# Performance work log

Hardware: AMD Instinct MI355X
Metric: run time of the kernel (lower is better)

Reference implementation:

```python
import itertools
import jax, jax.numpy as jnp
import numpy as np

GAMMA = 1.0

def setup_inputs() -> dict:
    key = jax.random.key(0)
    ks = jax.random.split(key, 11)
    B, T, NP, NG, J, H = 16, 32, 8, 4, 14, 256
    return {
        'hor_heatmap': jax.random.normal(ks[0], (B, T, 1, H, H), jnp.float32),
        'hor_offset': jax.random.normal(ks[1], (B, T, NP, 2), jnp.float32),
        'hor_bsize': jax.random.normal(ks[2], (B, T, NP, 4), jnp.float32),
        'hor_center': jax.random.normal(ks[3], (B, T, NP, 2), jnp.float32),
        'scores': jax.random.uniform(ks[4], (B, T, NP), jnp.float32),
        'x_pose3d': jax.random.normal(ks[5], (B, T, NP, J, 3), jnp.float32),
        'gt_heatmap': jax.random.normal(ks[6], (B, T, H, H), jnp.float32),
        'gt_hor_boxes_wh': jax.random.normal(ks[7], (B, T, NG, 4), jnp.float32),
        'gt_hor_offset': jax.random.normal(ks[8], (B, T, NG, 2), jnp.float32),
        'gt_hor_center': jax.random.normal(ks[9], (B, T, NG, 2), jnp.float32),
        'gt_pose3d': jax.random.normal(ks[10], (B, T, NG, J, 3), jnp.float32),
    }

def _make_perms(num_pred, num_gt):
    # all injective assignments of each gt column to a distinct pred row
    return np.asarray(list(itertools.permutations(range(num_pred), num_gt)), dtype=np.int32)

def _match(cost, perms):
    # cost: [NP, NG]; perms: [P, NG] static. Exact linear_sum_assignment by enumeration.
    ng = cost.shape[1]
    totals = cost[perms, jnp.arange(ng)].sum(-1)  # [P]
    return perms[jnp.argmin(totals)]              # rows matched to cols 0..NG-1

def reference(hor_heatmap, hor_offset, hor_bsize, hor_center, scores, x_pose3d,
              gt_heatmap, gt_hor_boxes_wh, gt_hor_offset, gt_hor_center, gt_pose3d):
    B, T, NP, _ = hor_center.shape
    NG = gt_hor_center.shape[2]
    J = x_pose3d.shape[3]
    BT = B * T
    perms = jnp.asarray(_make_perms(NP, NG))

    # center loss: MSE mean over full heatmaps
    center_loss = jnp.mean((hor_heatmap[:, :, 0] - gt_heatmap) ** 2)

    # --- Hungarian box/offset losses, vmapped over (b,t) ---
    def per_bt_box(pc, gc, sc, po, go, ps, gs):
        # cost[i,j] = -score[i] + ||pc_i - gc_j||
        C = jnp.linalg.norm(pc[:, None] - gc[None], axis=-1) - sc[:, None]  # [NP,NG]
        rows = _match(C, perms)                                             # [NG]
        off = jnp.mean(jnp.abs(po[rows] - go), axis=-1).sum()   # L1 mean per pair, summed
        size = jnp.mean(jnp.abs(ps[rows] - gs), axis=-1).sum()
        return off, size

    flat = lambda x: x.reshape((BT,) + x.shape[2:])
    offs, sizes = jax.vmap(per_bt_box)(
        flat(hor_center), flat(gt_hor_center), flat(scores),
        flat(hor_offset), flat(gt_hor_offset), flat(hor_bsize), flat(gt_hor_boxes_wh))
    total_offset_loss = offs.sum() / BT
    total_size_loss = sizes.sum() / BT

    # --- Hungarian pose loss ---
    def per_bt_pose(pp, gp):
        d = pp[:, None] - gp[None]                       # [NP,NG,J,3]
        C = jnp.sqrt(jnp.sum(d * d, axis=(-1, -2)))      # Frobenius norm cost
        rows = _match(C, perms)
        return jnp.sum((pp[rows] - gp) ** 2)             # MSE(sum) per pair, summed

    pose_loss = jax.vmap(per_bt_pose)(flat(x_pose3d), flat(gt_pose3d)).sum() / (BT * NP * J)

    detection_loss = center_loss + total_offset_loss + total_size_loss
    return GAMMA * detection_loss + pose_loss
```

## Files before the change

### kernel.cpp

```cpp
#include <hip/hip_runtime.h>

#define BT      512
#define NP      8
#define NG      4
#define JNT     14
#define NCENTER 33554432
#define NBLK_CENTER 1024

__global__ void init_ws_kernel(float* __restrict__ ws) {
    if (threadIdx.x < 4) ws[threadIdx.x] = 0.0f;
}

__global__ __launch_bounds__(256) void main_kernel(
    const float* __restrict__ hm,
    const float* __restrict__ hor_offset,
    const float* __restrict__ hor_bsize,
    const float* __restrict__ hor_center,
    const float* __restrict__ scores,
    const float* __restrict__ x_pose3d,
    const float* __restrict__ gt_hm,
    const float* __restrict__ gt_wh,
    const float* __restrict__ gt_off,
    const float* __restrict__ gt_center,
    const float* __restrict__ gt_pose,
    float* __restrict__ ws)
{
    __shared__ float sC[32];
    __shared__ float sCp[32];
    __shared__ float sv[8];
    __shared__ int   sp[8];

    const int blk = blockIdx.x;
    const int tid = threadIdx.x;

    if (blk < NBLK_CENTER) {
        const float4* a = (const float4*)hm;
        const float4* b = (const float4*)gt_hm;
        const int n4 = NCENTER / 4;
        float s = 0.0f;
        for (int i = blk * 256 + tid; i < n4; i += NBLK_CENTER * 256) {
            float4 x = a[i];
            float4 y = b[i];
            float d0 = x.x - y.x, d1 = x.y - y.y, d2 = x.z - y.z, d3 = x.w - y.w;
            s += d0 * d0 + d1 * d1 + d2 * d2 + d3 * d3;
        }
        #pragma unroll
        for (int o = 32; o > 0; o >>= 1) s += __shfl_down(s, o);
        const int lane = tid & 63, w = tid >> 6;
        if (lane == 0) sv[w] = s;
        __syncthreads();
        if (tid == 0) atomicAdd(&ws[0], sv[0] + sv[1] + sv[2] + sv[3]);
        return;
    }

    const int c = blk - NBLK_CENTER;
    const float* pc = hor_center + c * (NP * 2);
    const float* gc = gt_center  + c * (NG * 2);
    const float* sc = scores     + c * NP;
    const float* po = hor_offset + c * (NP * 2);
    const float* go = gt_off     + c * (NG * 2);
    const float* ps = hor_bsize  + c * (NP * 4);
    const float* gs = gt_wh      + c * (NG * 4);
    const float* pp = x_pose3d   + c * (NP * JNT * 3);
    const float* gp = gt_pose    + c * (NG * JNT * 3);

    if (tid < 32) {
        const int i = tid >> 2;
        const int j = tid & 3;
        float dx = pc[i * 2 + 0] - gc[j * 2 + 0];
        float dy = pc[i * 2 + 1] - gc[j * 2 + 1];
        sC[i * 4 + j] = sqrtf(dx * dx + dy * dy) - sc[i];
        float acc = 0.0f;
        const float* ai = pp + i * (JNT * 3);
        const float* gj = gp + j * (JNT * 3);
        #pragma unroll
        for (int k = 0; k < JNT * 3; k++) {
            float d = ai[k] - gj[k];
            acc += d * d;
        }
        sCp[i * 4 + j] = sqrtf(acc);
    }
    __syncthreads();

    float bv = 1e30f, bv2 = 1e30f;
    int bp = 0x7fffffff, bp2 = 0x7fffffff;
    for (int p = tid; p < 4096; p += 256) {
        const int i0 = (p >> 9) & 7, i1 = (p >> 6) & 7, i2 = (p >> 3) & 7, i3 = p & 7;
        if (i0 == i1 || i0 == i2 || i0 == i3 || i1 == i2 || i1 == i3 || i2 == i3) continue;
        float t  = sC [i0 * 4 + 0] + sC [i1 * 4 + 1] + sC [i2 * 4 + 2] + sC [i3 * 4 + 3];
        float t2 = sCp[i0 * 4 + 0] + sCp[i1 * 4 + 1] + sCp[i2 * 4 + 2] + sCp[i3 * 4 + 3];
        if (t  < bv)  { bv  = t;  bp  = p; }
        if (t2 < bv2) { bv2 = t2; bp2 = p; }
    }
    #pragma unroll
    for (int o = 32; o > 0; o >>= 1) {
        float v2 = __shfl_down(bv, o);  int p2 = __shfl_down(bp, o);
        if (v2 < bv  || (v2 == bv  && p2 < bp))  { bv  = v2; bp  = p2; }
        float w2 = __shfl_down(bv2, o); int q2 = __shfl_down(bp2, o);
        if (w2 < bv2 || (w2 == bv2 && q2 < bp2)) { bv2 = w2; bp2 = q2; }
    }
    const int lane = tid & 63, w = tid >> 6;
    if (lane == 0) { sv[w] = bv; sp[w] = bp; sv[4 + w] = bv2; sp[4 + w] = bp2; }
    __syncthreads();

    if (tid == 0) {
        for (int k = 1; k < 4; k++) {
            if (sv[k] < sv[0] || (sv[k] == sv[0] && sp[k] < sp[0])) { sv[0] = sv[k]; sp[0] = sp[k]; }
            if (sv[4 + k] < sv[4] || (sv[4 + k] == sv[4] && sp[4 + k] < sp[4])) { sv[4] = sv[4 + k]; sp[4] = sp[4 + k]; }
        }
        const int pb = sp[0];
        const int pq = sp[4];
        float off = 0.0f, size = 0.0f, pose = 0.0f;
        #pragma unroll
        for (int jj = 0; jj < 4; jj++) {
            const int r = (pb >> (9 - 3 * jj)) & 7;
            off += 0.5f * (fabsf(po[r * 2 + 0] - go[jj * 2 + 0]) +
                           fabsf(po[r * 2 + 1] - go[jj * 2 + 1]));
            size += 0.25f * (fabsf(ps[r * 4 + 0] - gs[jj * 4 + 0]) +
                             fabsf(ps[r * 4 + 1] - gs[jj * 4 + 1]) +
                             fabsf(ps[r * 4 + 2] - gs[jj * 4 + 2]) +
                             fabsf(ps[r * 4 + 3] - gs[jj * 4 + 3]));
            const int r2 = (pq >> (9 - 3 * jj)) & 7;
            const float* ai = pp + r2 * (JNT * 3);
            const float* gj = gp + jj * (JNT * 3);
            for (int k = 0; k < JNT * 3; k++) {
                float d = ai[k] - gj[k];
                pose += d * d;
            }
        }
        atomicAdd(&ws[1], off);
        atomicAdd(&ws[2], size);
        atomicAdd(&ws[3], pose);
    }
}

__global__ void final_kernel(const float* __restrict__ ws, float* __restrict__ out) {
    out[0] = ws[0] * (1.0f / (float)NCENTER)
           + (ws[1] + ws[2]) * (1.0f / (float)BT)
           + ws[3] * (1.0f / (float)(BT * NP * JNT));
}

extern "C" void kernel_launch(void* const* d_in, const int* in_sizes, int n_in,
                              void* d_out, int out_size, void* d_ws, size_t ws_size,
                              hipStream_t stream) {
    const float* hm         = (const float*)d_in[0];
    const float* hor_offset = (const float*)d_in[1];
    const float* hor_bsize  = (const float*)d_in[2];
    const float* hor_center = (const float*)d_in[3];
    const float* scores     = (const float*)d_in[4];
    const float* x_pose3d   = (const float*)d_in[5];
    const float* gt_hm      = (const float*)d_in[6];
    const float* gt_wh      = (const float*)d_in[7];
    const float* gt_off     = (const float*)d_in[8];
    const float* gt_center  = (const float*)d_in[9];
    const float* gt_pose    = (const float*)d_in[10];
    float* ws  = (float*)d_ws;
    float* out = (float*)d_out;

    init_ws_kernel<<<1, 64, 0, stream>>>(ws);
    main_kernel<<<NBLK_CENTER + BT, 256, 0, stream>>>(
        hm, hor_offset, hor_bsize, hor_center, scores, x_pose3d,
        gt_hm, gt_wh, gt_off, gt_center, gt_pose, ws);
    final_kernel<<<1, 1, 0, stream>>>(ws, out);
}
```

Baseline: 296.2 us.

## Use per-block partial sums with more center blocks and a fixed-trip unrolled loop

The center MSE pass now uses 4096 blocks instead of 1024, and each thread runs a fixed-count unrolled loop of 8 float4 loads so more loads are in flight. When the workspace is large enough, blocks write their partial sums to separate slots instead of doing atomics, and a 256-thread final kernel reduces them. This also removes the workspace-init launch. The atomic path stays as a fallback for small workspaces. The fixed trip count of 8 assumes the exact problem size.

```diff
diff --git a/kernel.cpp b/kernel.cpp
--- a/kernel.cpp
+++ b/kernel.cpp
@@ -5,11 +5,9 @@
 #define NG      4
 #define JNT     14
 #define NCENTER 33554432
-#define NBLK_CENTER 1024
-
-__global__ void init_ws_kernel(float* __restrict__ ws) {
-    if (threadIdx.x < 4) ws[threadIdx.x] = 0.0f;
-}
+#define NBLK_CENTER 4096
+#define WOFF    NBLK_CENTER
+
 
 __global__ __launch_bounds__(256) void main_kernel(
     const float* __restrict__ hm,
@@ -23,7 +21,8 @@
     const float* __restrict__ gt_off,
     const float* __restrict__ gt_center,
     const float* __restrict__ gt_pose,
-    float* __restrict__ ws)
+    float* __restrict__ ws,
+    int use_atomics)
 {
     __shared__ float sC[32];
     __shared__ float sCp[32];
@@ -36,9 +35,12 @@
     if (blk < NBLK_CENTER) {
         const float4* a = (const float4*)hm;
         const float4* b = (const float4*)gt_hm;
-        const int n4 = NCENTER / 4;
+        const int gsz  = NBLK_CENTER * 256;
+        const int base = blk * 256 + tid;
         float s = 0.0f;
-        for (int i = blk * 256 + tid; i < n4; i += NBLK_CENTER * 256) {
+        #pragma unroll 4
+        for (int k = 0; k < 8; k++) {
+            const int i = base + k * gsz;
             float4 x = a[i];
             float4 y = b[i];
             float d0 = x.x - y.x, d1 = x.y - y.y, d2 = x.z - y.z, d3 = x.w - y.w;
@@ -49,7 +51,11 @@
         const int lane = tid & 63, w = tid >> 6;
         if (lane == 0) sv[w] = s;
         __syncthreads();
-        if (tid == 0) atomicAdd(&ws[0], sv[0] + sv[1] + sv[2] + sv[3]);
+        if (tid == 0) {
+            float tot = sv[0] + sv[1] + sv[2] + sv[3];
+            if (use_atomics) atomicAdd(&ws[0], tot);
+            else             ws[blk] = tot;
+        }
         return;
     }
 
@@ -128,13 +134,59 @@
                 pose += d * d;
             }
         }
-        atomicAdd(&ws[1], off);
-        atomicAdd(&ws[2], size);
-        atomicAdd(&ws[3], pose);
-    }
-}
-
-__global__ void final_kernel(const float* __restrict__ ws, float* __restrict__ out) {
+        if (use_atomics) {
+            atomicAdd(&ws[1], off);
+            atomicAdd(&ws[2], size);
+            atomicAdd(&ws[3], pose);
+        } else {
+            float* slot = ws + WOFF + c * 4;
+            slot[0] = off;
+            slot[1] = size;
+            slot[2] = pose;
+        }
+    }
+}
+
+__global__ __launch_bounds__(256) void final_partials_kernel(
+    const float* __restrict__ ws, float* __restrict__ out)
+{
+    __shared__ float red[16];
+    const int tid = threadIdx.x;
+    float s0 = 0.0f, s1 = 0.0f, s2 = 0.0f, s3 = 0.0f;
+    for (int i = tid; i < NBLK_CENTER; i += 256) s0 += ws[i];
+    for (int c = tid; c < BT; c += 256) {
+        const float* slot = ws + WOFF + c * 4;
+        s1 += slot[0];
+        s2 += slot[1];
+        s3 += slot[2];
+    }
+    #pragma unroll
+    for (int o = 32; o > 0; o >>= 1) {
+        s0 += __shfl_down(s0, o);
+        s1 += __shfl_down(s1, o);
+        s2 += __shfl_down(s2, o);
+        s3 += __shfl_down(s3, o);
+    }
+    const int lane = tid & 63, w = tid >> 6;
+    if (lane == 0) { red[w] = s0; red[4 + w] = s1; red[8 + w] = s2; red[12 + w] = s3; }
+    __syncthreads();
+    if (tid == 0) {
+        s0 = red[0] + red[1] + red[2] + red[3];
+        s1 = red[4] + red[5] + red[6] + red[7];
+        s2 = red[8] + red[9] + red[10] + red[11];
+        s3 = red[12] + red[13] + red[14] + red[15];
+        out[0] = s0 * (1.0f / (float)NCENTER)
+               + (s1 + s2) * (1.0f / (float)BT)
+               + s3 * (1.0f / (float)(BT * NP * JNT));
+    }
+}
+
+
+__global__ void init_ws_kernel(float* __restrict__ ws) {
+    if (threadIdx.x < 4) ws[threadIdx.x] = 0.0f;
+}
+
+__global__ void final_atomic_kernel(const float* __restrict__ ws, float* __restrict__ out) {
     out[0] = ws[0] * (1.0f / (float)NCENTER)
            + (ws[1] + ws[2]) * (1.0f / (float)BT)
            + ws[3] * (1.0f / (float)(BT * NP * JNT));
@@ -157,9 +209,13 @@
     float* ws  = (float*)d_ws;
     float* out = (float*)d_out;
 
-    init_ws_kernel<<<1, 64, 0, stream>>>(ws);
+    const size_t needed = (size_t)(NBLK_CENTER + 4 * BT) * sizeof(float);
+    const int use_atomics = (ws_size < needed) ? 1 : 0;
+
+    if (use_atomics) init_ws_kernel<<<1, 64, 0, stream>>>(ws);
     main_kernel<<<NBLK_CENTER + BT, 256, 0, stream>>>(
         hm, hor_offset, hor_bsize, hor_center, scores, x_pose3d,
-        gt_hm, gt_wh, gt_off, gt_center, gt_pose, ws);
-    final_kernel<<<1, 1, 0, stream>>>(ws, out);
-}
+        gt_hm, gt_wh, gt_off, gt_center, gt_pose, ws, use_atomics);
+    if (use_atomics) final_atomic_kernel<<<1, 1, 0, stream>>>(ws, out);
+    else             final_partials_kernel<<<1, 256, 0, stream>>>(ws, out);
+}
```

Measured after the change: 308.6 us. +4.2%, slower.
